# Kernel optimization log

Measured on AMD Instinct MI355X. Metric: run time of the kernel, lower is better.

## Reference

```python
import jax, jax.numpy as jnp
import numpy as np

C1 = 0.01 ** 2
C2 = 0.03 ** 2
IN_CH = 3
WIN = 11
LEVELS = 5


def _gauss_kernel(k=WIN, sigma=1.5, c=IN_CH):
    ax = np.arange(k, dtype=np.float32) - (k - 1) / 2.0
    g = np.exp(-(ax ** 2) / (2.0 * sigma ** 2))
    g = g / g.sum()
    w2d = np.outer(g, g).astype(np.float32)  # [k,k]
    return jnp.asarray(np.tile(w2d[None, None], (c, 1, 1, 1)))  # [C,1,k,k]


def _dwconv(x, w):
    # depthwise (grouped) conv, 'same' padding for odd kernel
    pad = (w.shape[-1] - 1) // 2
    return jax.lax.conv_general_dilated(
        x, w, window_strides=(1, 1), padding=[(pad, pad), (pad, pad)],
        feature_group_count=x.shape[1],
        dimension_numbers=("NCHW", "OIHW", "NCHW"))


def _ssim_loss(i1, i2, w):
    m1 = _dwconv(i1, w)
    m2 = _dwconv(i2, w)
    m1sq = m1 * m1
    m2sq = m2 * m2
    m12 = m1 * m2
    s1 = _dwconv(i1 * i1, w) - m1sq
    s2 = _dwconv(i2 * i2, w) - m2sq
    s12 = _dwconv(i1 * i2, w) - m12
    ssim = (2 * m12 + C1) * (2 * s12 + C2) / ((m1sq + m2sq + C1) * (s1 + s2 + C2))
    return 1.0 - ssim.mean()


def _avg_pool2(x):
    B, C, H, W = x.shape
    return x.reshape(B, C, H // 2, 2, W // 2, 2).mean(axis=(3, 5))


def setup_inputs() -> dict:
    key = jax.random.key(0)
    k1, k2 = jax.random.split(key)
    img1 = jax.random.uniform(k1, (16, IN_CH, 512, 512), dtype=jnp.float32)
    img2 = jax.random.uniform(k2, (16, IN_CH, 512, 512), dtype=jnp.float32)
    inp = {"img1": img1, "img2": img2}
    for i in range(LEVELS):
        inp[f"g{i}"] = _gauss_kernel()
    return inp


def reference(img1, img2, g0, g1, g2, g3, g4):
    loss = jnp.asarray(0.0, dtype=img1.dtype)
    for w in (g0, g1, g2, g3, g4):
        loss = loss + _ssim_loss(img1, img2, w)
        img1 = _avg_pool2(img1)
        img2 = _avg_pool2(img2)
    return loss
```

## Files before the change

### kernel.cpp

```cpp
#include <hip/hip_runtime.h>
#include <math.h>

#define WIN 11
#define PAD 5
#define TW 64

typedef float v2f __attribute__((ext_vector_type(2)));

struct GW { float g[WIN]; };

template<bool EMIT>
__device__ __forceinline__ float ssim_wave_tile(
    const float* __restrict__ p1, const float* __restrict__ p2,
    int W, int X0, int Y0, const GW& gw, float2* __restrict__ rb,
    float* __restrict__ o1a, float* __restrict__ o1b, int Wout)
{
    const int TH = 32;
    const int lane = threadIdx.x & 63;
    const int gx = X0 + lane;
    const bool cval = gx < W;
    const int hx   = (lane < 5) ? (X0 - 5 + lane) : (X0 + 59 + lane);
    const bool hval = (lane < 10) && ((unsigned)hx < (unsigned)W);
    const int hpos = (lane < 5) ? lane : (64 + lane);
    const int cpos = 5 + lane;

    float vMp[11], vSp[11], vMq[11], vSq[11];
#pragma unroll
    for (int k = 0; k < 11; ++k) { vMp[k] = 0.f; vSp[k] = 0.f; vMq[k] = 0.f; vSq[k] = 0.f; }

    float part = 0.f;
    float pprev = 0.f, qprev = 0.f;

    auto LOAD = [&](int t, float& oa, float& ob, float& oah, float& obh) {
        int y = Y0 - PAD + t;
        oa = 0.f; ob = 0.f; oah = 0.f; obh = 0.f;
        if ((unsigned)y < (unsigned)W) {
            const float* r1 = p1 + (size_t)y * W;
            const float* r2 = p2 + (size_t)y * W;
            if (cval) { oa  = r1[gx]; ob  = r2[gx]; }
            if (hval) { oah = r1[hx]; obh = r2[hx]; }
        }
    };

    float a0, b0, ah0, bh0;
    float a1, b1, ah1, bh1;
    LOAD(0, a0, b0, ah0, bh0);
    LOAD(1, a1, b1, ah1, bh1);

#pragma unroll 1
    for (int blk = 0; blk < 4; ++blk) {
#pragma unroll
        for (int u = 0; u < 11; ++u) {
            const int t = blk * 11 + u;

            float a2, b2, ah2, bh2;
            LOAD(t + 2, a2, b2, ah2, bh2);

            float p = a0 + b0, q = a0 - b0;
            rb[cpos] = make_float2(p, q);
            if (lane < 10) {
                float ph = ah0 + bh0, qh = ah0 - bh0;
                rb[hpos] = make_float2(ph, qh);
            }
            __builtin_amdgcn_wave_barrier();

            v2f hM = {0.f, 0.f}, hS = {0.f, 0.f};
#pragma unroll
            for (int j = 0; j < WIN; ++j) {
                float2 v = rb[lane + j];
                v2f vm = { v.x, v.y };
                v2f g2 = { gw.g[j], gw.g[j] };
                hM = __builtin_elementwise_fma(g2, vm, hM);
                hS = __builtin_elementwise_fma(g2, vm * vm, hS);
            }
            __builtin_amdgcn_wave_barrier();
            float hp = hM.x, hq = hM.y, hpp = hS.x, hqq = hS.y;

#pragma unroll
            for (int s = 0; s < 11; ++s) {
                const int widx = 10 - ((s - u + 11) % 11);
                float g = gw.g[widx];
                vMp[s] = fmaf(g, hp,  vMp[s]);
                vSp[s] = fmaf(g, hpp, vSp[s]);
                vMq[s] = fmaf(g, hq,  vMq[s]);
                vSq[s] = fmaf(g, hqq, vSq[s]);
            }

            if (EMIT) {
                if (t >= 6 && t <= TH + 4 && (t & 1) == 0) {
                    float sp_ = p + pprev, sq_ = q + qprev;
                    float sp2 = sp_ + __shfl_down(sp_, 1, 64);
                    float sq2 = sq_ + __shfl_down(sq_, 1, 64);
                    if ((lane & 1) == 0) {
                        float P = sp2 * 0.25f, Q = sq2 * 0.25f;
                        int yo = (t - 6) >> 1;
                        size_t oo = (size_t)((Y0 >> 1) + yo) * Wout + ((X0 >> 1) + (lane >> 1));
                        o1a[oo] = (P + Q) * 0.5f;
                        o1b[oo] = (P - Q) * 0.5f;
                    }
                }
                pprev = p; qprev = q;
            }

            {
                int o = t - 10;
                if ((unsigned)o < (unsigned)TH) {
                    bool yok = (unsigned)(Y0 + o) < (unsigned)W;
                    float Mp = vMp[u], Sp_ = vSp[u], Mq = vMq[u], Sq_ = vSq[u];
                    const float C1v = 1e-4f, C2v = 9e-4f;
                    float A = Mp * Mp, B = Mq * Mq;
                    float ABp = A + B, ABm = A - B;
                    float SSp = Sp_ + Sq_, SSm = Sp_ - Sq_;
                    float n1 = fmaf(0.5f, ABm, C1v);
                    float n2 = fmaf(0.5f, SSm - ABm, C2v);
                    float e1 = fmaf(0.5f, ABp, C1v);
                    float e2 = fmaf(0.5f, SSp - ABp, C2v);
                    float v = (n1 * n2) * __builtin_amdgcn_rcpf(e1 * e2);
                    part += (cval && yok) ? v : 0.f;
                }
                vMp[u] = 0.f; vSp[u] = 0.f; vMq[u] = 0.f; vSq[u] = 0.f;
            }

            a0 = a1; b0 = b1; ah0 = ah1; bh0 = bh1;
            a1 = a2; b1 = b2; ah1 = ah2; bh1 = bh2;

            __builtin_amdgcn_sched_barrier(0);
        }
    }

    return part;
}

__global__ __launch_bounds__(256, 4) void ssim_l0_kernel(
    const float* __restrict__ i1, const float* __restrict__ i2,
    float* __restrict__ a1, float* __restrict__ b1,
    double* __restrict__ acc, GW gw)
{
    __shared__ float2 rbs[4][80];
    const int wid = threadIdx.x >> 6;
    const int w = blockIdx.x * 4 + wid;
    const int img = w >> 7;
    const int tt = w & 127;
    const int tx = tt & 7, ty = tt >> 3;
    const size_t off  = (size_t)img * 512 * 512;
    const size_t ooff = (size_t)img * 256 * 256;

    float part = ssim_wave_tile<true>(i1 + off, i2 + off, 512, tx * 64, ty * 32,
                                      gw, rbs[wid], a1 + ooff, b1 + ooff, 256);
#pragma unroll
    for (int o = 32; o > 0; o >>= 1) part += __shfl_down(part, o, 64);
    if ((threadIdx.x & 63) == 0) atomicAdd(acc, (double)part);
}

__global__ __launch_bounds__(256, 4) void ssim_rest_kernel(
    const float* __restrict__ a1, const float* __restrict__ b1,
    const float* __restrict__ a2, const float* __restrict__ b2,
    const float* __restrict__ a3, const float* __restrict__ b3,
    const float* __restrict__ a4, const float* __restrict__ b4,
    double* __restrict__ acc, GW gw)
{
    __shared__ float2 rbs[4][80];
    const int wid = threadIdx.x >> 6;
    const int w = blockIdx.x * 4 + wid;
    const int img = w / 43;
    const int r = w - img * 43;
    int lvl, tx, ty;
    if (r < 32)      { lvl = 1; tx = r & 3;  ty = r >> 2; }
    else if (r < 40) { lvl = 2; int s = r - 32; tx = s & 1; ty = s >> 1; }
    else if (r < 42) { lvl = 3; tx = 0; ty = r - 40; }
    else             { lvl = 4; tx = 0; ty = 0; }
    const int W = 512 >> lvl;
    const float* p1; const float* p2;
    switch (lvl) {
      case 1:  p1 = a1; p2 = b1; break;
      case 2:  p1 = a2; p2 = b2; break;
      case 3:  p1 = a3; p2 = b3; break;
      default: p1 = a4; p2 = b4; break;
    }
    const size_t off = (size_t)img * W * W;

    float part = ssim_wave_tile<false>(p1 + off, p2 + off, W, tx * 64, ty * 32,
                                       gw, rbs[wid], nullptr, nullptr, 0);
#pragma unroll
    for (int o = 32; o > 0; o >>= 1) part += __shfl_down(part, o, 64);
    if ((threadIdx.x & 63) == 0) atomicAdd(acc + lvl, (double)part);
}

__global__ __launch_bounds__(256) void pool_rest_kernel(
    const float* __restrict__ a1, const float* __restrict__ b1,
    float* __restrict__ a2, float* __restrict__ b2,
    float* __restrict__ a3, float* __restrict__ b3,
    float* __restrict__ a4, float* __restrict__ b4)
{
    __shared__ float l2[32][33];
    __shared__ float l3[16][17];
    const int tid = threadIdx.x;
    const int im = blockIdx.y;
    const int tb = blockIdx.x;
    const int tx = tb & 3, ty = tb >> 2;
    const bool second = im >= 48;
    const int ii = second ? im - 48 : im;
    const float* src = (second ? b1 : a1) + (size_t)ii * 256 * 256;
    float* o2 = (second ? b2 : a2) + (size_t)ii * 128 * 128;
    float* o3 = (second ? b3 : a3) + (size_t)ii * 64 * 64;
    float* o4 = (second ? b4 : a4) + (size_t)ii * 32 * 32;
    const int X0 = tx * 64, Y0 = ty * 64;

#pragma unroll
    for (int k = 0; k < 2; ++k) {
        int idx = tid + k * 256;
        int xp = idx & 15;
        int yo = idx >> 4;
        const float* rp = src + (size_t)(Y0 + 2 * yo) * 256 + (X0 + 4 * xp);
        float4 r0 = *(const float4*)rp;
        float4 r1 = *(const float4*)(rp + 256);
        float v0 = (r0.x + r0.y + r1.x + r1.y) * 0.25f;
        float v1 = (r0.z + r0.w + r1.z + r1.w) * 0.25f;
        l2[yo][2 * xp]     = v0;
        l2[yo][2 * xp + 1] = v1;
        float2* op = (float2*)(o2 + (size_t)((Y0 >> 1) + yo) * 128 + ((X0 >> 1) + 2 * xp));
        *op = make_float2(v0, v1);
    }
    __syncthreads();
    {
        int xo = tid & 15, yo = tid >> 4;
        if (yo < 16) {
            float v = (l2[2*yo][2*xo] + l2[2*yo][2*xo+1] +
                       l2[2*yo+1][2*xo] + l2[2*yo+1][2*xo+1]) * 0.25f;
            l3[yo][xo] = v;
            o3[(size_t)((Y0 >> 2) + yo) * 64 + ((X0 >> 2) + xo)] = v;
        }
    }
    __syncthreads();
    if (tid < 64) {
        int xo = tid & 7, yo = tid >> 3;
        float v = (l3[2*yo][2*xo] + l3[2*yo][2*xo+1] +
                   l3[2*yo+1][2*xo] + l3[2*yo+1][2*xo+1]) * 0.25f;
        o4[(size_t)((Y0 >> 3) + yo) * 32 + ((X0 >> 3) + xo)] = v;
    }
}

__global__ void final_kernel(const double* __restrict__ acc, float* __restrict__ out)
{
    double loss = 0.0;
#pragma unroll
    for (int l = 0; l < 5; ++l) {
        double cnt = 48.0 * (double)(512 >> l) * (double)(512 >> l);
        loss += 1.0 - acc[l] / cnt;
    }
    out[0] = (float)loss;
}

extern "C" void kernel_launch(void* const* d_in, const int* in_sizes, int n_in,
                              void* d_out, int out_size, void* d_ws, size_t ws_size,
                              hipStream_t stream)
{
    const float* img1 = (const float*)d_in[0];
    const float* img2 = (const float*)d_in[1];
    float* out = (float*)d_out;

    GW gw;
    double gs[WIN], sum = 0.0;
    for (int i = 0; i < WIN; ++i) {
        double ax = (double)i - 5.0;
        gs[i] = exp(-(ax * ax) / 4.5);
        sum += gs[i];
    }
    for (int i = 0; i < WIN; ++i) gw.g[i] = (float)(gs[i] / sum);

    double* acc = (double*)d_ws;
    float* base = (float*)((char*)d_ws + 64);
    const size_t n1 = 48ull * 256 * 256;
    const size_t n2 = 48ull * 128 * 128;
    const size_t n3 = 48ull * 64 * 64;
    const size_t n4 = 48ull * 32 * 32;
    float* a1 = base;      float* b1 = a1 + n1;
    float* a2 = b1 + n1;   float* b2 = a2 + n2;
    float* a3 = b2 + n2;   float* b3 = a3 + n3;
    float* a4 = b3 + n3;   float* b4 = a4 + n4;

    hipMemsetAsync(acc, 0, 5 * sizeof(double), stream);

    hipLaunchKernelGGL(ssim_l0_kernel, dim3(1536), dim3(256), 0, stream,
                       img1, img2, a1, b1, acc, gw);

    hipLaunchKernelGGL(pool_rest_kernel, dim3(16, 96), dim3(256), 0, stream,
                       a1, b1, a2, b2, a3, b3, a4, b4);

    hipLaunchKernelGGL(ssim_rest_kernel, dim3(516), dim3(256), 0, stream,
                       a1, b1, a2, b2, a3, b3, a4, b4, acc, gw);

    hipLaunchKernelGGL(final_kernel, dim3(1), dim3(1), 0, stream, acc, out);
}
```

Measured before the change: 277.9 us.

## Process two rows per step with float4 LDS ring and 12-slot vertical accumulators

Restructures the per-wave sliding-window SSIM loop to handle two input rows per step. It packs both rows' sum/difference pairs into one float4 LDS write and read, halving the number of LDS round-trips and wave barriers. The vertical accumulators move to a 12-slot packed v2f ring, and loads become unconditional with clamped indices plus selects instead of branches. The cost is more live registers for the accumulators and row buffers, with a possible occupancy risk under launch_bounds(256,4). It also computes 42 rows instead of 44, and the pooled-output emit logic has to be rewritten to match.

```diff
diff --git a/kernel.cpp b/kernel.cpp
--- a/kernel.cpp
+++ b/kernel.cpp
@@ -3,130 +3,181 @@
 
 #define WIN 11
 #define PAD 5
-#define TW 64
 
 typedef float v2f __attribute__((ext_vector_type(2)));
 
 struct GW { float g[WIN]; };
+
+
+struct TileCtx {
+    const float* p1; const float* p2;
+    float* o1a; float* o1b;
+    int W, X0, Y0, Wout;
+    int lane, cpos, wpos, gxc, hxc;
+    bool cval, hval;
+};
+
+__device__ __forceinline__ void load_row(const TileCtx& c, int t,
+    float& oa, float& ob, float& oah, float& obh)
+{
+    int y = c.Y0 - PAD + t;
+    bool yin = (unsigned)y < (unsigned)c.W;
+    const float* r1 = c.p1 + (size_t)(yin ? y : 0) * c.W;
+    const float* r2 = c.p2 + (size_t)(yin ? y : 0) * c.W;
+    float va = r1[c.gxc], vb = r2[c.gxc];
+    float wa = r1[c.hxc], wb = r2[c.hxc];
+    bool cv = yin && c.cval;
+    bool hv = yin && c.hval;
+    oa  = cv ? va : 0.f;
+    ob  = cv ? vb : 0.f;
+    oah = hv ? wa : 0.f;
+    obh = hv ? wb : 0.f;
+}
+
+__device__ __forceinline__ void emit_one(const TileCtx& cx, v2f M, v2f S,
+                                         int o, float& part)
+{
+    const int TH = 32;
+    if ((unsigned)o < (unsigned)TH) {
+        bool yok = (unsigned)(cx.Y0 + o) < (unsigned)cx.W;
+        float Mp = M.x, Mq = M.y, Sp_ = S.x, Sq_ = S.y;
+        const float C1v = 1e-4f, C2v = 9e-4f;
+        float A = Mp * Mp, B = Mq * Mq;
+        float ABp = A + B, ABm = A - B;
+        float SSp = Sp_ + Sq_, SSm = Sp_ - Sq_;
+        float n1 = fmaf(0.5f, ABm, C1v);
+        float n2 = fmaf(0.5f, SSm - ABm, C2v);
+        float e1 = fmaf(0.5f, ABp, C1v);
+        float e2 = fmaf(0.5f, SSp - ABp, C2v);
+        float val = (n1 * n2) * __builtin_amdgcn_rcpf(e1 * e2);
+        part += (cx.cval && yok) ? val : 0.f;
+    }
+}
+
+template<int U, bool EMIT>
+__device__ __forceinline__ void ssim_step(
+    const TileCtx& cx, const GW& gw, float4* __restrict__ rb, int d,
+    float (&cur)[8], v2f (&vM)[12], v2f (&vS)[12],
+    float& part, float& pprev, float& qprev)
+{
+    float n0, n1, n2, n3, n4, n5, n6, n7;
+    load_row(cx, 2 * d + 2, n0, n1, n2, n3);
+    load_row(cx, 2 * d + 3, n4, n5, n6, n7);
+
+    float p0  = cur[0] + cur[1], q0  = cur[0] - cur[1];
+    float ph0 = cur[2] + cur[3], qh0 = cur[2] - cur[3];
+    float p1r = cur[4] + cur[5], q1r = cur[4] - cur[5];
+    float ph1 = cur[6] + cur[7], qh1 = cur[6] - cur[7];
+    rb[cx.cpos] = make_float4(p0, q0, p1r, q1r);
+    rb[cx.wpos] = (cx.lane < 10) ? make_float4(ph0, qh0, ph1, qh1)
+                                 : make_float4(p0, q0, p1r, q1r);
+    __builtin_amdgcn_wave_barrier();
+
+    v2f hM0 = {0.f, 0.f}, hS0 = {0.f, 0.f};
+    v2f hM1 = {0.f, 0.f}, hS1 = {0.f, 0.f};
+#pragma unroll
+    for (int j = 0; j < WIN; ++j) {
+        float4 vv = rb[cx.lane + j];
+        v2f v0 = { vv.x, vv.y }, v1 = { vv.z, vv.w };
+        v2f g2 = { gw.g[j], gw.g[j] };
+        hM0 = __builtin_elementwise_fma(g2, v0, hM0);
+        hS0 = __builtin_elementwise_fma(g2, v0 * v0, hS0);
+        hM1 = __builtin_elementwise_fma(g2, v1, hM1);
+        hS1 = __builtin_elementwise_fma(g2, v1 * v1, hS1);
+    }
+    __builtin_amdgcn_wave_barrier();
+
+#pragma unroll
+    for (int s = 0; s < 12; ++s) {
+        const int w0v = ((2 * U - s) % 12 + 12) % 12;
+        if (w0v <= 10) {
+            v2f g2 = { gw.g[w0v], gw.g[w0v] };
+            vM[s] = __builtin_elementwise_fma(g2, hM0, vM[s]);
+            vS[s] = __builtin_elementwise_fma(g2, hS0, vS[s]);
+        }
+        const int w1v = (w0v + 1) % 12;
+        if (w1v <= 10) {
+            v2f g2 = { gw.g[w1v], gw.g[w1v] };
+            vM[s] = __builtin_elementwise_fma(g2, hM1, vM[s]);
+            vS[s] = __builtin_elementwise_fma(g2, hS1, vS[s]);
+        }
+    }
+
+    {
+        const int s0 = (2 * U + 2) % 12;
+        const int s1 = (2 * U + 3) % 12;
+        emit_one(cx, vM[s0], vS[s0], 2 * d - 10, part);
+        emit_one(cx, vM[s1], vS[s1], 2 * d - 9,  part);
+        vM[s0] = (v2f){0.f, 0.f}; vS[s0] = (v2f){0.f, 0.f};
+        vM[s1] = (v2f){0.f, 0.f}; vS[s1] = (v2f){0.f, 0.f};
+    }
+
+    if (EMIT) {
+        int r_ = 2 * d;
+        if (r_ >= 6 && r_ <= 36) {
+            float sp_ = p0 + pprev, sq_ = q0 + qprev;
+            float sp2 = sp_ + __shfl_down(sp_, 1, 64);
+            float sq2 = sq_ + __shfl_down(sq_, 1, 64);
+            if ((cx.lane & 1) == 0) {
+                float P = sp2 * 0.25f, Q = sq2 * 0.25f;
+                int yo = d - 3;
+                size_t oo = (size_t)((cx.Y0 >> 1) + yo) * cx.Wout
+                          + ((cx.X0 >> 1) + (cx.lane >> 1));
+                cx.o1a[oo] = (P + Q) * 0.5f;
+                cx.o1b[oo] = (P - Q) * 0.5f;
+            }
+        }
+        pprev = p1r; qprev = q1r;
+    }
+
+    cur[0] = n0; cur[1] = n1; cur[2] = n2; cur[3] = n3;
+    cur[4] = n4; cur[5] = n5; cur[6] = n6; cur[7] = n7;
+
+    __builtin_amdgcn_sched_barrier(0);
+}
 
 template<bool EMIT>
 __device__ __forceinline__ float ssim_wave_tile(
     const float* __restrict__ p1, const float* __restrict__ p2,
-    int W, int X0, int Y0, const GW& gw, float2* __restrict__ rb,
+    int W, int X0, int Y0, const GW& gw, float4* __restrict__ rb,
     float* __restrict__ o1a, float* __restrict__ o1b, int Wout)
 {
-    const int TH = 32;
-    const int lane = threadIdx.x & 63;
-    const int gx = X0 + lane;
-    const bool cval = gx < W;
-    const int hx   = (lane < 5) ? (X0 - 5 + lane) : (X0 + 59 + lane);
-    const bool hval = (lane < 10) && ((unsigned)hx < (unsigned)W);
-    const int hpos = (lane < 5) ? lane : (64 + lane);
-    const int cpos = 5 + lane;
-
-    float vMp[11], vSp[11], vMq[11], vSq[11];
-#pragma unroll
-    for (int k = 0; k < 11; ++k) { vMp[k] = 0.f; vSp[k] = 0.f; vMq[k] = 0.f; vSq[k] = 0.f; }
-
-    float part = 0.f;
-    float pprev = 0.f, qprev = 0.f;
-
-    auto LOAD = [&](int t, float& oa, float& ob, float& oah, float& obh) {
-        int y = Y0 - PAD + t;
-        oa = 0.f; ob = 0.f; oah = 0.f; obh = 0.f;
-        if ((unsigned)y < (unsigned)W) {
-            const float* r1 = p1 + (size_t)y * W;
-            const float* r2 = p2 + (size_t)y * W;
-            if (cval) { oa  = r1[gx]; ob  = r2[gx]; }
-            if (hval) { oah = r1[hx]; obh = r2[hx]; }
-        }
-    };
-
-    float a0, b0, ah0, bh0;
-    float a1, b1, ah1, bh1;
-    LOAD(0, a0, b0, ah0, bh0);
-    LOAD(1, a1, b1, ah1, bh1);
+    TileCtx cx;
+    cx.p1 = p1; cx.p2 = p2; cx.o1a = o1a; cx.o1b = o1b;
+    cx.W = W; cx.X0 = X0; cx.Y0 = Y0; cx.Wout = Wout;
+    cx.lane = threadIdx.x & 63;
+    const int gx = X0 + cx.lane;
+    cx.cval = gx < W;
+    const int hx = (cx.lane < 5) ? (X0 - 5 + cx.lane) : (X0 + 59 + cx.lane);
+    cx.hval = (cx.lane < 10) && ((unsigned)hx < (unsigned)W);
+    const int hpos = (cx.lane < 5) ? cx.lane : (64 + cx.lane);
+    cx.cpos = 5 + cx.lane;
+    cx.gxc = cx.cval ? gx : 0;
+    cx.hxc = cx.hval ? hx : cx.gxc;
+    cx.wpos = (cx.lane < 10) ? hpos : cx.cpos;
+
+    v2f vM[12], vS[12];
+#pragma unroll
+    for (int k = 0; k < 12; ++k) { vM[k] = (v2f){0.f, 0.f}; vS[k] = (v2f){0.f, 0.f}; }
+
+    float part = 0.f, pprev = 0.f, qprev = 0.f;
+    float cur[8];
+    load_row(cx, 0, cur[0], cur[1], cur[2], cur[3]);
+    load_row(cx, 1, cur[4], cur[5], cur[6], cur[7]);
 
 #pragma unroll 1
-    for (int blk = 0; blk < 4; ++blk) {
-#pragma unroll
-        for (int u = 0; u < 11; ++u) {
-            const int t = blk * 11 + u;
-
-            float a2, b2, ah2, bh2;
-            LOAD(t + 2, a2, b2, ah2, bh2);
-
-            float p = a0 + b0, q = a0 - b0;
-            rb[cpos] = make_float2(p, q);
-            if (lane < 10) {
-                float ph = ah0 + bh0, qh = ah0 - bh0;
-                rb[hpos] = make_float2(ph, qh);
-            }
-            __builtin_amdgcn_wave_barrier();
-
-            v2f hM = {0.f, 0.f}, hS = {0.f, 0.f};
-#pragma unroll
-            for (int j = 0; j < WIN; ++j) {
-                float2 v = rb[lane + j];
-                v2f vm = { v.x, v.y };
-                v2f g2 = { gw.g[j], gw.g[j] };
-                hM = __builtin_elementwise_fma(g2, vm, hM);
-                hS = __builtin_elementwise_fma(g2, vm * vm, hS);
-            }
-            __builtin_amdgcn_wave_barrier();
-            float hp = hM.x, hq = hM.y, hpp = hS.x, hqq = hS.y;
-
-#pragma unroll
-            for (int s = 0; s < 11; ++s) {
-                const int widx = 10 - ((s - u + 11) % 11);
-                float g = gw.g[widx];
-                vMp[s] = fmaf(g, hp,  vMp[s]);
-                vSp[s] = fmaf(g, hpp, vSp[s]);
-                vMq[s] = fmaf(g, hq,  vMq[s]);
-                vSq[s] = fmaf(g, hqq, vSq[s]);
-            }
-
-            if (EMIT) {
-                if (t >= 6 && t <= TH + 4 && (t & 1) == 0) {
-                    float sp_ = p + pprev, sq_ = q + qprev;
-                    float sp2 = sp_ + __shfl_down(sp_, 1, 64);
-                    float sq2 = sq_ + __shfl_down(sq_, 1, 64);
-                    if ((lane & 1) == 0) {
-                        float P = sp2 * 0.25f, Q = sq2 * 0.25f;
-                        int yo = (t - 6) >> 1;
-                        size_t oo = (size_t)((Y0 >> 1) + yo) * Wout + ((X0 >> 1) + (lane >> 1));
-                        o1a[oo] = (P + Q) * 0.5f;
-                        o1b[oo] = (P - Q) * 0.5f;
-                    }
-                }
-                pprev = p; qprev = q;
-            }
-
-            {
-                int o = t - 10;
-                if ((unsigned)o < (unsigned)TH) {
-                    bool yok = (unsigned)(Y0 + o) < (unsigned)W;
-                    float Mp = vMp[u], Sp_ = vSp[u], Mq = vMq[u], Sq_ = vSq[u];
-                    const float C1v = 1e-4f, C2v = 9e-4f;
-                    float A = Mp * Mp, B = Mq * Mq;
-                    float ABp = A + B, ABm = A - B;
-                    float SSp = Sp_ + Sq_, SSm = Sp_ - Sq_;
-                    float n1 = fmaf(0.5f, ABm, C1v);
-                    float n2 = fmaf(0.5f, SSm - ABm, C2v);
-                    float e1 = fmaf(0.5f, ABp, C1v);
-                    float e2 = fmaf(0.5f, SSp - ABp, C2v);
-                    float v = (n1 * n2) * __builtin_amdgcn_rcpf(e1 * e2);
-                    part += (cval && yok) ? v : 0.f;
-                }
-                vMp[u] = 0.f; vSp[u] = 0.f; vMq[u] = 0.f; vSq[u] = 0.f;
-            }
-
-            a0 = a1; b0 = b1; ah0 = ah1; bh0 = bh1;
-            a1 = a2; b1 = b2; ah1 = ah2; bh1 = bh2;
-
-            __builtin_amdgcn_sched_barrier(0);
-        }
-    }
+    for (int blk = 0; blk < 3; ++blk) {
+        const int db = blk * 6;
+        ssim_step<0, EMIT>(cx, gw, rb, db + 0, cur, vM, vS, part, pprev, qprev);
+        ssim_step<1, EMIT>(cx, gw, rb, db + 1, cur, vM, vS, part, pprev, qprev);
+        ssim_step<2, EMIT>(cx, gw, rb, db + 2, cur, vM, vS, part, pprev, qprev);
+        ssim_step<3, EMIT>(cx, gw, rb, db + 3, cur, vM, vS, part, pprev, qprev);
+        ssim_step<4, EMIT>(cx, gw, rb, db + 4, cur, vM, vS, part, pprev, qprev);
+        ssim_step<5, EMIT>(cx, gw, rb, db + 5, cur, vM, vS, part, pprev, qprev);
+    }
+    ssim_step<0, EMIT>(cx, gw, rb, 18, cur, vM, vS, part, pprev, qprev);
+    ssim_step<1, EMIT>(cx, gw, rb, 19, cur, vM, vS, part, pprev, qprev);
+    ssim_step<2, EMIT>(cx, gw, rb, 20, cur, vM, vS, part, pprev, qprev);
 
     return part;
 }
@@ -136,7 +187,7 @@
     float* __restrict__ a1, float* __restrict__ b1,
     double* __restrict__ acc, GW gw)
 {
-    __shared__ float2 rbs[4][80];
+    __shared__ float4 rbs[4][80];
     const int wid = threadIdx.x >> 6;
     const int w = blockIdx.x * 4 + wid;
     const int img = w >> 7;
@@ -159,7 +210,7 @@
     const float* __restrict__ a4, const float* __restrict__ b4,
     double* __restrict__ acc, GW gw)
 {
-    __shared__ float2 rbs[4][80];
+    __shared__ float4 rbs[4][80];
     const int wid = threadIdx.x >> 6;
     const int w = blockIdx.x * 4 + wid;
     const int img = w / 43;
```

After: 340.1 us. 22.4% more time.
